# Kernel tuning notes

Measured on AMD Instinct MI355X. Metric: run time of the kernel, lower is better.

The kernel has to match this reference:

```python
import jax, jax.numpy as jnp
import numpy as np

B, N, D, H = 8, 1024, 768, 12
HD = D // H  # 64


def setup_inputs() -> dict:
    key = jax.random.key(0)
    ks = jax.random.split(key, 10)
    input_graph = jax.random.normal(ks[0], (B, N, D), dtype=jnp.float32)
    u = jax.random.uniform(ks[1], (B, N, N), dtype=jnp.float32)
    keep = jax.random.uniform(ks[2], (B, N, N)) < 0.15
    adj = jnp.where(keep, u, 0.0)
    s = 1.0 / np.sqrt(D)
    Wq = jax.random.normal(ks[3], (D, D), dtype=jnp.float32) * s
    bq = jnp.zeros((D,), dtype=jnp.float32)
    Wk = jax.random.normal(ks[4], (D, D), dtype=jnp.float32) * s
    bk = jnp.zeros((D,), dtype=jnp.float32)
    Wv = jax.random.normal(ks[5], (D, D), dtype=jnp.float32) * s
    bv = jnp.zeros((D,), dtype=jnp.float32)
    beta = jnp.asarray(0.1, dtype=jnp.float32)
    return {"input_graph": input_graph, "adj": adj, "Wq": Wq, "bq": bq,
            "Wk": Wk, "bk": bk, "Wv": Wv, "bv": bv, "beta": beta}


def _split_heads(x):
    # [B,N,D] -> [B,H,N,HD]
    b, n, _ = x.shape
    return x.reshape(b, n, H, HD).transpose(0, 2, 1, 3)


def reference(input_graph, adj, Wq, bq, Wk, bk, Wv, bv, beta):
    q = _split_heads(input_graph @ Wq + bq)  # [B,H,N,HD]
    k = _split_heads(input_graph @ Wk + bk)
    v = _split_heads(input_graph @ Wv + bv)
    scores = jnp.einsum('bhqd,bhkd->bhqk', q, k) / jnp.sqrt(jnp.asarray(HD, input_graph.dtype))
    adj_e = adj[:, None, :, :]  # [B,1,N,N]
    scores = scores + beta * adj_e
    scores = jnp.where(adj_e > 0, scores, jnp.asarray(-9e15, scores.dtype))
    probs = jax.nn.softmax(scores, axis=-1)
    out = jnp.einsum('bhqk,bhkd->bhqd', probs, v)  # [B,H,N,HD]
    return out.transpose(0, 2, 1, 3).reshape(input_graph.shape[0], input_graph.shape[1], D)
```

## Files before the change

kernel.cpp:

```cpp
#include <hip/hip_runtime.h>

#define B_ 8
#define N_ 1024
#define D_ 768
#define H_ 12
#define HD_ 64

#define LOG2E 1.4426950408889634f

typedef __attribute__((ext_vector_type(8))) short bf16x8;
typedef __attribute__((ext_vector_type(4))) short short4_t;
typedef __attribute__((ext_vector_type(4))) float f32x4;
typedef __attribute__((ext_vector_type(2))) unsigned int u32x2;
typedef unsigned int u32;

__device__ __forceinline__ short f2bf(float f) {
  union { float f; unsigned u; } v; v.f = f;
  unsigned u = v.u;
  unsigned r = u + 0x7fffu + ((u >> 16) & 1u);
  return (short)(r >> 16);
}
__device__ __forceinline__ float bf2f(short s) {
  union { unsigned u; float f; } v;
  v.u = ((unsigned)(unsigned short)s) << 16;
  return v.f;
}
__device__ __forceinline__ float bpermf(int srclane, float x) {
  union { float f; int i; } v; v.f = x;
  union { int i; float f; } r;
  r.i = __builtin_amdgcn_ds_bpermute(srclane * 4, v.i);
  return r.f;
}
__device__ __forceinline__ float max3f(float a, float b, float c) {
  return fmaxf(fmaxf(a, b), c);
}
__device__ __forceinline__ u32 cvtpk(float a, float b) {
  u32 r;
  asm("v_cvt_pk_bf16_f32 %0, %1, %2" : "=v"(r) : "v"(a), "v"(b));
  return r;
}

__device__ __forceinline__ void gload_lds16(const void* g, void* l) {
  __builtin_amdgcn_global_load_lds((const __attribute__((address_space(1))) u32*)g,
                                   (__attribute__((address_space(3))) u32*)l, 16, 0, 0);
}

__global__ void cvt_x_kernel(const float* __restrict__ X, short* __restrict__ Xb) {
  int i = (blockIdx.x * 256 + threadIdx.x) * 8;
  float4 a = *(const float4*)(X + i);
  float4 b = *(const float4*)(X + i + 4);
  bf16x8 o;
  o[0] = f2bf(a.x); o[1] = f2bf(a.y); o[2] = f2bf(a.z); o[3] = f2bf(a.w);
  o[4] = f2bf(b.x); o[5] = f2bf(b.y); o[6] = f2bf(b.z); o[7] = f2bf(b.w);
  *(bf16x8*)(Xb + i) = o;
}

__global__ void cvt_w_kernel(const float* __restrict__ Wq, const float* __restrict__ Wk,
                             const float* __restrict__ Wv, short* __restrict__ Wt3) {
  const float* W = blockIdx.z == 0 ? Wq : (blockIdx.z == 1 ? Wk : Wv);
  short* O = Wt3 + (size_t)blockIdx.z * D_ * D_;
  __shared__ float t[32][33];
  int n0 = blockIdx.x * 32, k0 = blockIdx.y * 32;
  int tx = threadIdx.x, ty = threadIdx.y;
#pragma unroll
  for (int j = 0; j < 4; j++)
    t[ty + 8 * j][tx] = W[(size_t)(k0 + ty + 8 * j) * D_ + n0 + tx];
  __syncthreads();
#pragma unroll
  for (int j = 0; j < 4; j++)
    O[(size_t)(n0 + ty + 8 * j) * D_ + k0 + tx] = f2bf(t[tx][ty + 8 * j]);
}

__global__ __launch_bounds__(256)
void madj_kernel(const float* __restrict__ adj, const float* __restrict__ beta_p,
                 short* __restrict__ madjF) {
  const int qt = blockIdx.x, kt = blockIdx.y, b = blockIdx.z;
  const int tid = threadIdx.x;
  const float b2 = beta_p[0] * LOG2E;
  const float MASKV = -9.0e15f * LOG2E;

  __shared__ float Lt[64][68];
  {
    const int row = tid >> 2, cs = (tid & 3) * 16;
    const float* ap = adj + ((size_t)b * N_ + qt * 64 + row) * (size_t)N_ + kt * 64 + cs;
#pragma unroll
    for (int j = 0; j < 4; j++)
      *(float4*)&Lt[row][cs + 4 * j] = *(const float4*)(ap + 4 * j);
  }
  __syncthreads();

  const int lane = tid & 63, w = tid >> 6;
  const int l15 = lane & 15, lg = lane >> 4;
  const int q = 16 * w + l15;
  short vals[16];
#pragma unroll
  for (int cb = 0; cb < 4; cb++) {
    float4 a4 = *(const float4*)&Lt[q][16 * cb + 4 * lg];
    float av[4] = {a4.x, a4.y, a4.z, a4.w};
#pragma unroll
    for (int r = 0; r < 4; r++) {
      float a = av[r];
      vals[cb * 4 + r] = f2bf((a > 0.f) ? b2 * a : MASKV);
    }
  }
  short* o = madjF + (((size_t)(b * 16 + qt) * 16 + kt) * 256 + tid) * 16;
  bf16x8 lo, hi;
#pragma unroll
  for (int j = 0; j < 8; j++) { lo[j] = vals[j]; hi[j] = vals[8 + j]; }
  *(bf16x8*)o = lo;
  *(bf16x8*)(o + 8) = hi;
}

__global__ __launch_bounds__(256, 4)
void qkv_gemm_kernel(const short* __restrict__ Xb, const short* __restrict__ Wt3,
                     const float* __restrict__ bq, const float* __restrict__ bk,
                     const float* __restrict__ bv, short* __restrict__ QKV) {
  const int z = blockIdx.z;
  const short* Wt = Wt3 + (size_t)z * D_ * D_;
  const float* bias = z == 0 ? bq : (z == 1 ? bk : bv);
  short* C = QKV + (size_t)z * (B_ * N_) * D_;
  const float alpha = (z == 0) ? 0.125f * LOG2E : 1.0f;

  const int m0 = blockIdx.x * 128;
  const int n0 = blockIdx.y * 128;
  const int tid = threadIdx.x;
  const int lane = tid & 63;
  const int wid = tid >> 6;
  const int wr = (wid >> 1) * 64;
  const int wc = (wid & 1) * 64;
  const int l15 = lane & 15;
  const int lg = lane >> 4;

  __shared__ short At[2][128][32];
  __shared__ short Bt[2][128][32];

  f32x4 acc[4][4];
#pragma unroll
  for (int m = 0; m < 4; m++)
#pragma unroll
    for (int n = 0; n < 4; n++)
      acc[m][n] = (f32x4){0.f, 0.f, 0.f, 0.f};

  const int srow_l = lane >> 2;
  const int sc8 = (((lane & 3) ^ ((lane >> 2) & 3)) * 8);
  const short* ag = Xb + (size_t)(m0 + wid * 16 + srow_l) * D_ + sc8;
  const short* bg = Wt + (size_t)(n0 + wid * 16 + srow_l) * D_ + sc8;

  auto stage = [&](int bi, int k0) {
#pragma unroll
    for (int p = 0; p < 2; p++) {
      gload_lds16(ag + (size_t)(64 * p) * D_ + k0,
                  ((short*)At[bi]) + (size_t)(wid + 4 * p) * 512);
      gload_lds16(bg + (size_t)(64 * p) * D_ + k0,
                  ((short*)Bt[bi]) + (size_t)(wid + 4 * p) * 512);
    }
  };

  stage(0, 0);
  for (int k0 = 0; k0 < D_; k0 += 32) {
    const int cur = (k0 >> 5) & 1;
    __syncthreads();
    if (k0 + 32 < D_) stage(cur ^ 1, k0 + 32);

    bf16x8 af[4], bfr[4];
#pragma unroll
    for (int m = 0; m < 4; m++) {
      const int row = wr + m * 16 + l15;
      af[m] = *(const bf16x8*)&At[cur][row][(lg ^ (l15 & 3)) * 8];
    }
#pragma unroll
    for (int n = 0; n < 4; n++) {
      const int row = wc + n * 16 + l15;
      bfr[n] = *(const bf16x8*)&Bt[cur][row][(lg ^ (l15 & 3)) * 8];
    }
#pragma unroll
    for (int m = 0; m < 4; m++)
#pragma unroll
      for (int n = 0; n < 4; n++)
        acc[m][n] = __builtin_amdgcn_mfma_f32_16x16x32_bf16(af[m], bfr[n], acc[m][n], 0, 0, 0);
  }

#pragma unroll
  for (int n = 0; n < 4; n++) {
    const int col = n0 + wc + n * 16 + l15;
    const float bval = bias[col];
#pragma unroll
    for (int m = 0; m < 4; m++) {
#pragma unroll
      for (int r = 0; r < 4; r++) {
        const int row = m0 + wr + m * 16 + 4 * lg + r;
        C[(size_t)row * D_ + col] = f2bf((acc[m][n][r] + bval) * alpha);
      }
    }
  }
}

__global__ __launch_bounds__(256)
void vT_kernel(const short* __restrict__ Vb, short* __restrict__ VTg) {
  const int nt = blockIdx.x, h = blockIdx.y, b = blockIdx.z;
  const int tid = threadIdx.x;
  __shared__ short st[64][68];
  const int n0 = nt * 64;
  {
    const int row = tid >> 2, c = (tid & 3) * 16;
    const short* p = Vb + ((size_t)b * N_ + n0 + row) * D_ + h * HD_ + c;
    *(bf16x8*)&st[row][c] = *(const bf16x8*)p;
    *(bf16x8*)&st[row][c + 8] = *(const bf16x8*)(p + 8);
  }
  __syncthreads();
  {
    const int d = tid >> 2, nb = (tid & 3) * 16;
    bf16x8 o0, o1;
#pragma unroll
    for (int i = 0; i < 8; i++) { o0[i] = st[nb + i][d]; o1[i] = st[nb + 8 + i][d]; }
    short* q = VTg + ((size_t)(b * H_ + h) * HD_ + d) * N_ + n0 + nb;
    *(bf16x8*)q = o0;
    *(bf16x8*)(q + 8) = o1;
  }
}

__global__ __launch_bounds__(256, 4)
void attn_kernel(const short* __restrict__ QKV, const short* __restrict__ VTg,
                 const short* __restrict__ madjF, float* __restrict__ out) {
  const short* Qb = QKV;
  const short* Kb = QKV + (size_t)(B_ * N_) * D_;

  const int wg = blockIdx.x;
  const int swz = (wg & 7) * 192 + (wg >> 3);
  const int qt = swz & 15;
  const int h = (swz >> 4) % 12;
  const int b = swz / 192;

  const int tid = threadIdx.x;
  const int lane = tid & 63;
  const int w = tid >> 6;
  const int l15 = lane & 15;
  const int lg = lane >> 4;

  const int q0 = qt * 64;
  const size_t seq0 = (size_t)b * N_;
  const int hc = h * HD_;

  __shared__ short Kt[2][64][64];
  __shared__ short VTt[2][64][64];
  __shared__ short Pt[4][16][64];

  bf16x8 qf[2];
  {
    const short* qp = Qb + (seq0 + q0 + 16 * w + l15) * (size_t)D_ + hc + 8 * lg;
    qf[0] = *(const bf16x8*)qp;
    qf[1] = *(const bf16x8*)(qp + 32);
  }

  f32x4 acc[4];
#pragma unroll
  for (int cb = 0; cb < 4; cb++) acc[cb] = (f32x4){0.f, 0.f, 0.f, 0.f};
  float m_ = -__builtin_inff();
  float l_ = 0.f;

  const int krow = 16 * w + (lane >> 3);
  const int kc8 = ((lane & 7) ^ (lane >> 3)) * 8;
  const short* kg = Kb + (seq0 + krow) * (size_t)D_ + hc + kc8;
  const short* vg = VTg + ((size_t)(b * H_ + h) * HD_ + krow) * N_ + kc8;
  const short* mg = madjF + ((size_t)(b * 16 + qt) * 16) * 4096 + tid * 16;

  const int sw2 = (l15 & 7) << 1;
  char* ptrow = (char*)&Pt[w][l15][0];

  auto stage = [&](int bi, int kt) {
    const int k0 = kt * 64;
    gload_lds16(kg + (size_t)k0 * D_, ((short*)Kt[bi]) + (size_t)w * 1024);
    gload_lds16(kg + (size_t)(k0 + 8) * D_, ((short*)Kt[bi]) + (size_t)w * 1024 + 512);
    gload_lds16(vg + k0, ((short*)VTt[bi]) + (size_t)w * 1024);
    gload_lds16(vg + k0 + 8 * (size_t)N_, ((short*)VTt[bi]) + (size_t)w * 1024 + 512);
  };

  stage(0, 0);
  bf16x8 mlo = *(const bf16x8*)mg;
  bf16x8 mhi = *(const bf16x8*)(mg + 8);

  for (int kt = 0; kt < 16; kt++) {
    const int cur = kt & 1;
    __syncthreads();
    if (kt < 15) stage(cur ^ 1, kt + 1);
    const int ktn = kt < 15 ? kt + 1 : 15;
    bf16x8 mlo2 = *(const bf16x8*)(mg + (size_t)ktn * 4096);
    bf16x8 mhi2 = *(const bf16x8*)(mg + (size_t)ktn * 4096 + 8);

    f32x4 s[4];
#pragma unroll
    for (int cb = 0; cb < 4; cb++) {
      f32x4 c;
#pragma unroll
      for (int r = 0; r < 4; r++)
        c[r] = bf2f(cb < 2 ? mlo[(cb & 1) * 4 + r] : mhi[(cb & 1) * 4 + r]);
      const int swk = l15 & 7;
      bf16x8 kf0 = *(const bf16x8*)&Kt[cur][cb * 16 + l15][(lg ^ swk) * 8];
      bf16x8 kf1 = *(const bf16x8*)&Kt[cur][cb * 16 + l15][((lg + 4) ^ swk) * 8];
      c = __builtin_amdgcn_mfma_f32_16x16x32_bf16(kf0, qf[0], c, 0, 0, 0);
      s[cb] = __builtin_amdgcn_mfma_f32_16x16x32_bf16(kf1, qf[1], c, 0, 0, 0);
    }
    mlo = mlo2; mhi = mhi2;

    float tm = max3f(max3f(s[0][0], s[0][1], s[0][2]),
                     max3f(s[0][3], s[1][0], s[1][1]),
                     max3f(s[1][2], s[1][3], s[2][0]));
    float tm2 = max3f(max3f(s[2][1], s[2][2], s[2][3]),
                      max3f(s[3][0], s[3][1], s[3][2]), s[3][3]);
    tm = fmaxf(tm, tm2);
    tm = fmaxf(tm, __shfl_xor(tm, 16));
    tm = fmaxf(tm, __shfl_xor(tm, 32));

    if (!__all(tm <= m_ + 8.f)) {
      const float mnew = fmaxf(m_, tm);
      const float sc2 = __builtin_exp2f(m_ - mnew);
      m_ = mnew;
      l_ *= sc2;
      float scr[4];
#pragma unroll
      for (int r = 0; r < 4; r++) scr[r] = bpermf(4 * lg + r, sc2);
#pragma unroll
      for (int cb = 0; cb < 4; cb++)
#pragma unroll
        for (int r = 0; r < 4; r++) acc[cb][r] *= scr[r];
    }

    float ps = 0.f;
    u32 pk[8];
#pragma unroll
    for (int cb = 0; cb < 4; cb++) {
#pragma unroll
      for (int rp = 0; rp < 2; rp++) {
        const float p0 = __builtin_exp2f(s[cb][2 * rp] - m_);
        const float p1 = __builtin_exp2f(s[cb][2 * rp + 1] - m_);
        ps += p0 + p1;
        pk[cb * 2 + rp] = cvtpk(p0, p1);
      }
    }
    ps += __shfl_xor(ps, 16);
    ps += __shfl_xor(ps, 32);
    l_ += ps;

#pragma unroll
    for (int cb = 0; cb < 4; cb++) {
      u32x2 wv = {pk[2 * cb], pk[2 * cb + 1]};
      *(u32x2*)(ptrow + (((4 * cb + lg) ^ sw2) << 3)) = wv;
    }

#pragma unroll
    for (int ks = 0; ks < 2; ks++) {
      bf16x8 pa = *(const bf16x8*)(ptrow + ((((lg << 1) + 8 * ks) ^ sw2) << 3));
#pragma unroll
      for (int cb = 0; cb < 4; cb++) {
        const int row = cb * 16 + l15;
        bf16x8 vb = *(const bf16x8*)&VTt[cur][row][((lg + 4 * ks) ^ (row & 7)) * 8];
        acc[cb] = __builtin_amdgcn_mfma_f32_16x16x32_bf16(pa, vb, acc[cb], 0, 0, 0);
      }
    }
  }

  float inv[4];
#pragma unroll
  for (int r = 0; r < 4; r++) inv[r] = 1.f / bpermf(4 * lg + r, l_);
#pragma unroll
  for (int cb = 0; cb < 4; cb++) {
#pragma unroll
    for (int r = 0; r < 4; r++) {
      out[(seq0 + q0 + 16 * w + 4 * lg + r) * (size_t)D_ + hc + cb * 16 + l15] =
          acc[cb][r] * inv[r];
    }
  }
}

extern "C" void kernel_launch(void* const* d_in, const int* in_sizes, int n_in,
                              void* d_out, int out_size, void* d_ws, size_t ws_size,
                              hipStream_t stream) {
  const float* X    = (const float*)d_in[0];
  const float* adj  = (const float*)d_in[1];
  const float* Wq   = (const float*)d_in[2];
  const float* bq   = (const float*)d_in[3];
  const float* Wk   = (const float*)d_in[4];
  const float* bk   = (const float*)d_in[5];
  const float* Wv   = (const float*)d_in[6];
  const float* bv   = (const float*)d_in[7];
  const float* beta = (const float*)d_in[8];
  float* out = (float*)d_out;

  short* Xb    = (short*)d_ws;
  short* Wt3   = Xb + (size_t)(B_ * N_) * D_;
  short* QKV   = Wt3 + 3 * (size_t)D_ * D_;
  short* madjF = QKV + 3 * (size_t)(B_ * N_) * D_;
  short* VTg   = Xb;

  cvt_x_kernel<<<dim3((B_ * N_ * D_) / (256 * 8)), 256, 0, stream>>>(X, Xb);
  cvt_w_kernel<<<dim3(24, 24, 3), dim3(32, 8), 0, stream>>>(Wq, Wk, Wv, Wt3);
  madj_kernel<<<dim3(16, 16, 8), 256, 0, stream>>>(adj, beta, madjF);
  qkv_gemm_kernel<<<dim3(64, 6, 3), 256, 0, stream>>>(Xb, Wt3, bq, bk, bv, QKV);
  vT_kernel<<<dim3(16, 12, 8), 256, 0, stream>>>(QKV + 2 * (size_t)(B_ * N_) * D_, VTg);
  attn_kernel<<<dim3(1536), 256, 0, stream>>>(QKV, VTg, madjF, out);
}
```

Baseline: 131.2 us.

## Fuse V transpose into QKV GEMM epilogue and double attention tile to 128 queries

The QKV GEMM epilogue now writes V directly in per-head transposed [B,H,HD,N] layout with 4-wide bf16 stores, so the separate vT_kernel launch and its round trip through global memory go away. The attention kernel moves to 512-thread blocks covering 128 query rows with 8 waves, which halves the block count and lets each staged K/V tile be shared by twice as many waves, with one load per thread instead of two. The block index mapping also changes to put batch in the low bits. The transposed-V stores are strided 8-byte writes, and the larger blocks may lower occupancy.

```diff
diff --git a/kernel.cpp b/kernel.cpp
--- a/kernel.cpp
+++ b/kernel.cpp
@@ -180,56 +180,51 @@
         acc[m][n] = __builtin_amdgcn_mfma_f32_16x16x32_bf16(af[m], bfr[n], acc[m][n], 0, 0, 0);
   }
 
-#pragma unroll
-  for (int n = 0; n < 4; n++) {
-    const int col = n0 + wc + n * 16 + l15;
-    const float bval = bias[col];
-#pragma unroll
-    for (int m = 0; m < 4; m++) {
-#pragma unroll
-      for (int r = 0; r < 4; r++) {
-        const int row = m0 + wr + m * 16 + 4 * lg + r;
-        C[(size_t)row * D_ + col] = f2bf((acc[m][n][r] + bval) * alpha);
+  if (z == 2) {
+#pragma unroll
+    for (int n = 0; n < 4; n++) {
+      const int col = n0 + wc + n * 16 + l15;
+      const float bval = bias[col];
+      const int hh = col >> 6, dd = col & 63;
+#pragma unroll
+      for (int m = 0; m < 4; m++) {
+        const int row = m0 + wr + m * 16 + 4 * lg;
+        const int bb = row >> 10, nn = row & 1023;
+        short4_t o;
+#pragma unroll
+        for (int r = 0; r < 4; r++) o[r] = f2bf(acc[m][n][r] + bval);
+        *(short4_t*)&C[(((size_t)bb * H_ + hh) * HD_ + dd) * N_ + nn] = o;
       }
     }
-  }
-}
-
-__global__ __launch_bounds__(256)
-void vT_kernel(const short* __restrict__ Vb, short* __restrict__ VTg) {
-  const int nt = blockIdx.x, h = blockIdx.y, b = blockIdx.z;
-  const int tid = threadIdx.x;
-  __shared__ short st[64][68];
-  const int n0 = nt * 64;
-  {
-    const int row = tid >> 2, c = (tid & 3) * 16;
-    const short* p = Vb + ((size_t)b * N_ + n0 + row) * D_ + h * HD_ + c;
-    *(bf16x8*)&st[row][c] = *(const bf16x8*)p;
-    *(bf16x8*)&st[row][c + 8] = *(const bf16x8*)(p + 8);
-  }
-  __syncthreads();
-  {
-    const int d = tid >> 2, nb = (tid & 3) * 16;
-    bf16x8 o0, o1;
-#pragma unroll
-    for (int i = 0; i < 8; i++) { o0[i] = st[nb + i][d]; o1[i] = st[nb + 8 + i][d]; }
-    short* q = VTg + ((size_t)(b * H_ + h) * HD_ + d) * N_ + n0 + nb;
-    *(bf16x8*)q = o0;
-    *(bf16x8*)(q + 8) = o1;
-  }
-}
-
-__global__ __launch_bounds__(256, 4)
-void attn_kernel(const short* __restrict__ QKV, const short* __restrict__ VTg,
-                 const short* __restrict__ madjF, float* __restrict__ out) {
+  } else {
+#pragma unroll
+    for (int n = 0; n < 4; n++) {
+      const int col = n0 + wc + n * 16 + l15;
+      const float bval = bias[col];
+#pragma unroll
+      for (int m = 0; m < 4; m++) {
+#pragma unroll
+        for (int r = 0; r < 4; r++) {
+          const int row = m0 + wr + m * 16 + 4 * lg + r;
+          C[(size_t)row * D_ + col] = f2bf((acc[m][n][r] + bval) * alpha);
+        }
+      }
+    }
+  }
+}
+
+__global__ __launch_bounds__(512, 4)
+void attn_kernel(const short* __restrict__ QKV, const short* __restrict__ madjF,
+                 float* __restrict__ out) {
   const short* Qb = QKV;
   const short* Kb = QKV + (size_t)(B_ * N_) * D_;
+  const short* VTg = QKV + 2 * (size_t)(B_ * N_) * D_;
 
   const int wg = blockIdx.x;
-  const int swz = (wg & 7) * 192 + (wg >> 3);
-  const int qt = swz & 15;
-  const int h = (swz >> 4) % 12;
-  const int b = swz / 192;
+  const int b = wg & 7;
+  const int rem = wg >> 3;
+  const int h = rem >> 3;
+  const int qt = rem & 7;
 
   const int tid = threadIdx.x;
   const int lane = tid & 63;
@@ -237,13 +232,13 @@
   const int l15 = lane & 15;
   const int lg = lane >> 4;
 
-  const int q0 = qt * 64;
+  const int q0 = qt * 128;
   const size_t seq0 = (size_t)b * N_;
   const int hc = h * HD_;
 
   __shared__ short Kt[2][64][64];
   __shared__ short VTt[2][64][64];
-  __shared__ short Pt[4][16][64];
+  __shared__ short Pt[8][16][64];
 
   bf16x8 qf[2];
   {
@@ -258,21 +253,20 @@
   float m_ = -__builtin_inff();
   float l_ = 0.f;
 
-  const int krow = 16 * w + (lane >> 3);
-  const int kc8 = ((lane & 7) ^ (lane >> 3)) * 8;
-  const short* kg = Kb + (seq0 + krow) * (size_t)D_ + hc + kc8;
-  const short* vg = VTg + ((size_t)(b * H_ + h) * HD_ + krow) * N_ + kc8;
-  const short* mg = madjF + ((size_t)(b * 16 + qt) * 16) * 4096 + tid * 16;
+  const int srow = 8 * w + (lane >> 3);
+  const int sc8 = ((lane & 7) ^ (lane >> 3)) * 8;
+  const short* kg = Kb + (seq0 + srow) * (size_t)D_ + hc + sc8;
+  const short* vg = VTg + ((size_t)(b * H_ + h) * HD_ + srow) * N_ + sc8;
+  const int qm = 2 * qt + (w >> 2);
+  const short* mg = madjF + ((size_t)(b * 16 + qm) * 16) * 4096 + ((w & 3) * 64 + lane) * 16;
 
   const int sw2 = (l15 & 7) << 1;
   char* ptrow = (char*)&Pt[w][l15][0];
 
   auto stage = [&](int bi, int kt) {
     const int k0 = kt * 64;
-    gload_lds16(kg + (size_t)k0 * D_, ((short*)Kt[bi]) + (size_t)w * 1024);
-    gload_lds16(kg + (size_t)(k0 + 8) * D_, ((short*)Kt[bi]) + (size_t)w * 1024 + 512);
-    gload_lds16(vg + k0, ((short*)VTt[bi]) + (size_t)w * 1024);
-    gload_lds16(vg + k0 + 8 * (size_t)N_, ((short*)VTt[bi]) + (size_t)w * 1024 + 512);
+    gload_lds16(kg + (size_t)k0 * D_, ((short*)Kt[bi]) + (size_t)w * 512);
+    gload_lds16(vg + k0, ((short*)VTt[bi]) + (size_t)w * 512);
   };
 
   stage(0, 0);
@@ -390,12 +384,10 @@
   short* Wt3   = Xb + (size_t)(B_ * N_) * D_;
   short* QKV   = Wt3 + 3 * (size_t)D_ * D_;
   short* madjF = QKV + 3 * (size_t)(B_ * N_) * D_;
-  short* VTg   = Xb;
 
   cvt_x_kernel<<<dim3((B_ * N_ * D_) / (256 * 8)), 256, 0, stream>>>(X, Xb);
   cvt_w_kernel<<<dim3(24, 24, 3), dim3(32, 8), 0, stream>>>(Wq, Wk, Wv, Wt3);
   madj_kernel<<<dim3(16, 16, 8), 256, 0, stream>>>(adj, beta, madjF);
   qkv_gemm_kernel<<<dim3(64, 6, 3), 256, 0, stream>>>(Xb, Wt3, bq, bk, bv, QKV);
-  vT_kernel<<<dim3(16, 12, 8), 256, 0, stream>>>(QKV + 2 * (size_t)(B_ * N_) * D_, VTg);
-  attn_kernel<<<dim3(1536), 256, 0, stream>>>(QKV, VTg, madjF, out);
-}
+  attn_kernel<<<dim3(768), 512, 0, stream>>>(QKV, madjF, out);
+}
```

Result: faster. 127.1 us (-3.1%).
